# Performance work log

Measured on AMD Instinct MI355X. Metric: run time of the kernel, lower is better.

## Reference

```python
import jax, jax.numpy as jnp
import numpy as np
import math

DIM = 2048
N_HEADS = 32
N_KV_HEADS = 8
HEAD_DIM = DIM // N_HEADS  # 64
N_REP = N_HEADS // N_KV_HEADS  # 4
BSZ, SEQ = 2, 2048


def setup_inputs() -> dict:
    key = jax.random.key(0)
    ks = jax.random.split(key, 8)
    x = jax.random.normal(ks[0], (BSZ, SEQ, DIM), dtype=jnp.float32)
    # rotary tables, [seq, head_dim//2]
    inv_freq = 1.0 / (10000.0 ** (np.arange(0, HEAD_DIM, 2, dtype=np.float32) / HEAD_DIM))
    t = np.arange(SEQ, dtype=np.float32)
    freqs = np.outer(t, inv_freq)
    freqs_cos = jnp.asarray(np.cos(freqs))
    freqs_sin = jnp.asarray(np.sin(freqs))
    s = 0.02
    wq = jax.random.normal(ks[1], (DIM, N_HEADS * HEAD_DIM), dtype=jnp.float32) * s
    wk = jax.random.normal(ks[2], (DIM, N_KV_HEADS * HEAD_DIM), dtype=jnp.float32) * s
    wv = jax.random.normal(ks[3], (DIM, N_KV_HEADS * HEAD_DIM), dtype=jnp.float32) * s
    wo = jax.random.normal(ks[4], (N_HEADS * HEAD_DIM, DIM), dtype=jnp.float32) * s
    return {"x": x, "freqs_cos": freqs_cos, "freqs_sin": freqs_sin,
            "wq": wq, "wk": wk, "wv": wv, "wo": wo}


def _apply_rotary(xq, xk, cos, sin):
    # xq: [b,s,h,d], xk: [b,s,kh,d]; cos/sin: [s, d//2]
    def rot(t):
        tr = t[..., 0::2]  # even -> real
        ti = t[..., 1::2]  # odd  -> imag
        c = cos[None, :, None, :]
        s_ = sin[None, :, None, :]
        or_ = tr * c - ti * s_
        oi_ = tr * s_ + ti * c
        # interleave back: [..., d//2, 2] -> [..., d]
        return jnp.stack([or_, oi_], axis=-1).reshape(t.shape)
    return rot(xq), rot(xk)


def reference(x, freqs_cos, freqs_sin, wq, wk, wv, wo):
    b, s, _ = x.shape
    xq = (x @ wq).reshape(b, s, N_HEADS, HEAD_DIM)
    xk = (x @ wk).reshape(b, s, N_KV_HEADS, HEAD_DIM)
    xv = (x @ wv).reshape(b, s, N_KV_HEADS, HEAD_DIM)
    xq, xk = _apply_rotary(xq, xk, freqs_cos, freqs_sin)
    # repeat_kv: [b,s,kh,d] -> [b,s,kh*n_rep,d]
    xk = jnp.repeat(xk, N_REP, axis=2)
    xv = jnp.repeat(xv, N_REP, axis=2)
    # [b,h,s,d]
    q = xq.transpose(0, 2, 1, 3)
    k = xk.transpose(0, 2, 1, 3)
    v = xv.transpose(0, 2, 1, 3)
    scale = 1.0 / math.sqrt(HEAD_DIM)
    scores = jnp.einsum('bhqd,bhkd->bhqk', q, k) * scale
    causal = jnp.tril(jnp.ones((s, s), dtype=bool))
    scores = jnp.where(causal[None, None], scores, jnp.float32(-jnp.inf))
    probs = jax.nn.softmax(scores, axis=-1)
    out = jnp.einsum('bhqk,bhkd->bhqd', probs, v)  # [b,h,s,d]
    out = out.transpose(0, 2, 1, 3).reshape(b, s, N_HEADS * HEAD_DIM)
    return out @ wo
```

## Files before the change

kernel.cpp:

```cpp
#include <hip/hip_runtime.h>
#include <hip/hip_bf16.h>

typedef __attribute__((ext_vector_type(8))) short short8;
typedef __attribute__((ext_vector_type(4))) float f32x4;

__device__ __forceinline__ unsigned short f2bf(float f) {
  union { float f; unsigned u; } v; v.f = f;
  unsigned r = v.u + 0x7FFFu + ((v.u >> 16) & 1u);
  return (unsigned short)(r >> 16);
}
__device__ __forceinline__ float bf2f(unsigned short h) {
  union { unsigned u; float f; } v; v.u = ((unsigned)h) << 16;
  return v.f;
}
__device__ __forceinline__ unsigned pkbf(float a, float b) {
  __hip_bfloat162 h = __float22bfloat162_rn(float2{a, b});
  union { __hip_bfloat162 h; unsigned u; } cv; cv.h = h;
  return cv.u;
}

__global__ void prep(const float* __restrict__ x, const float* __restrict__ wq,
                     const float* __restrict__ wk, const float* __restrict__ wv,
                     const float* __restrict__ wo, unsigned short* __restrict__ xb,
                     unsigned short* __restrict__ wt, unsigned short* __restrict__ wot) {
  const int z = blockIdx.z, tid = threadIdx.x;
  if (z == 0) {
    int id = blockIdx.y * 64 + blockIdx.x;
#pragma unroll
    for (int rep = 0; rep < 2; ++rep) {
      int i = (rep * 4096 + id) * 256 + tid;
      float4 v = ((const float4*)x)[i];
      ushort4 o;
      o.x = f2bf(v.x); o.y = f2bf(v.y); o.z = f2bf(v.z); o.w = f2bf(v.w);
      ((ushort4*)xb)[i] = o;
    }
    return;
  }
  __shared__ float tile[32][33];
  const float* src;
  unsigned short* dst;
  int N;
  if (z == 1) { src = wq; dst = wt; N = 2048; }
  else if (z == 2) { src = wk; dst = wt + 2048ull * 2048; N = 512; }
  else if (z == 3) { src = wv; dst = wt + 2560ull * 2048; N = 512; }
  else { src = wo; dst = wot; N = 2048; }
  const int K = 2048;
  int n0 = blockIdx.x * 32, k0 = blockIdx.y * 32;
  if (n0 >= N) return;
  int xx = tid & 31, yy = tid >> 5;
#pragma unroll
  for (int j = 0; j < 4; ++j) tile[yy + 8 * j][xx] = src[(size_t)(k0 + yy + 8 * j) * N + n0 + xx];
  __syncthreads();
#pragma unroll
  for (int j = 0; j < 4; ++j) dst[(size_t)(n0 + yy + 8 * j) * K + k0 + xx] = f2bf(tile[xx][yy + 8 * j]);
}

template <int MODE>
__global__ __launch_bounds__(256, 2) void gemm_bt64(const unsigned short* __restrict__ A,
                                                    const unsigned short* __restrict__ Bt,
                                                    void* __restrict__ Cv, int K, int ldc,
                                                    unsigned short* __restrict__ vt,
                                                    const float* __restrict__ fcos,
                                                    const float* __restrict__ fsin) {
  __shared__ alignas(16) unsigned short As[128 * 64];
  __shared__ alignas(16) unsigned short Bs[128 * 64];
  const int t = threadIdx.x;
  const int lane = t & 63, w = t >> 6;
  const int l15 = lane & 15, quad = lane >> 4;
  const int bn0 = blockIdx.x * 128, bm0 = blockIdx.y * 128;
  const int wm = (w >> 1) * 64, wn = (w & 1) * 64;
  const unsigned short* Ab = A + (size_t)bm0 * K;
  const unsigned short* Bb = Bt + (size_t)bn0 * K;
  const int asw = l15 & 7;

  f32x4 acc[4][4];
  const f32x4 zf = {0.f, 0.f, 0.f, 0.f};
#pragma unroll
  for (int i = 0; i < 4; ++i)
#pragma unroll
    for (int j = 0; j < 4; ++j) acc[i][j] = zf;

  for (int k0 = 0; k0 < K; k0 += 64) {
    __syncthreads();
#pragma unroll
    for (int r = 0; r < 4; ++r) {
      int e = r * 256 + t;
      int row = e >> 3, cslot = e & 7;
      int cg = cslot ^ (row & 7);
      const unsigned short* ga = Ab + (size_t)row * K + k0 + cg * 8;
      __builtin_amdgcn_global_load_lds((const __attribute__((address_space(1))) void*)ga,
                                       (__attribute__((address_space(3))) void*)(As + e * 8), 16, 0, 0);
      const unsigned short* gb = Bb + (size_t)row * K + k0 + cg * 8;
      __builtin_amdgcn_global_load_lds((const __attribute__((address_space(1))) void*)gb,
                                       (__attribute__((address_space(3))) void*)(Bs + e * 8), 16, 0, 0);
    }
    __syncthreads();
#pragma unroll
    for (int s = 0; s < 2; ++s) {
      short8 af[4], bf[4];
#pragma unroll
      for (int i = 0; i < 4; ++i)
        af[i] = *reinterpret_cast<const short8*>(As + (wm + i * 16 + l15) * 64 + (((s * 4 + quad) ^ asw) * 8));
#pragma unroll
      for (int j = 0; j < 4; ++j)
        bf[j] = *reinterpret_cast<const short8*>(Bs + (wn + j * 16 + l15) * 64 + (((s * 4 + quad) ^ asw) * 8));
      __builtin_amdgcn_s_setprio(1);
#pragma unroll
      for (int i = 0; i < 4; ++i)
#pragma unroll
        for (int j = 0; j < 4; ++j)
          acc[i][j] = __builtin_amdgcn_mfma_f32_16x16x32_bf16(af[i], bf[j], acc[i][j], 0, 0, 0);
      __builtin_amdgcn_s_setprio(0);
    }
  }

  if (MODE == 1 && bn0 >= 2560) {
    const int b = bm0 >> 11;
#pragma unroll
    for (int i = 0; i < 4; ++i) {
      int srow = (bm0 + wm + i * 16 + quad * 4) & 2047;
#pragma unroll
      for (int j = 0; j < 4; ++j) {
        int vcol = bn0 - 2560 + wn + j * 16 + l15;
        int kvh = vcol >> 6, d = vcol & 63;
        uint2 pk = make_uint2(pkbf(acc[i][j][0], acc[i][j][1]), pkbf(acc[i][j][2], acc[i][j][3]));
        *reinterpret_cast<uint2*>(vt + ((size_t)(b * 8 + kvh) * 64 + d) * 2048 + srow) = pk;
      }
    }
  } else if (MODE == 1 && bn0 >= 2048) {
#pragma unroll
    for (int i = 0; i < 4; ++i)
#pragma unroll
      for (int j = 0; j < 4; ++j)
#pragma unroll
        for (int r = 0; r < 4; ++r) {
          int row = bm0 + wm + i * 16 + quad * 4 + r;
          int s = row & 2047;
          int col = bn0 + wn + j * 16 + l15;
          int fi = ((col - 2048) >> 1) & 31;
          float val = acc[i][j][r];
          float par = __shfl_xor(val, 1, 64);
          float c = fcos[s * 32 + fi], sn = fsin[s * 32 + fi];
          float o = (lane & 1) ? (par * sn + val * c) : (val * c - par * sn);
          ((unsigned short*)Cv)[(size_t)row * ldc + col] = f2bf(o);
        }
  } else {
#pragma unroll
    for (int i = 0; i < 4; ++i)
#pragma unroll
      for (int j = 0; j < 4; ++j)
#pragma unroll
        for (int r = 0; r < 4; ++r) {
          size_t row = (size_t)(bm0 + wm + i * 16 + quad * 4 + r);
          size_t col = (size_t)(bn0 + wn + j * 16 + l15);
          if (MODE == 1)
            ((unsigned short*)Cv)[row * ldc + col] = f2bf(acc[i][j][r]);
          else
            ((float*)Cv)[row * ldc + col] = acc[i][j][r];
        }
  }
}

__global__ __launch_bounds__(256, 4) void flash_attn(const unsigned short* __restrict__ qkv,
                                                     const unsigned short* __restrict__ vt,
                                                     const float* __restrict__ fcos,
                                                     const float* __restrict__ fsin,
                                                     unsigned short* __restrict__ out) {
  __shared__ alignas(16) unsigned short Ks[64 * 64];
  __shared__ alignas(16) unsigned short Vs[64 * 64];
  __shared__ alignas(16) unsigned short Ps[128 * 64];
  const int t = threadIdx.x, lane = t & 63, w = t >> 6;
  const int l15 = lane & 15, quad = lane >> 4;
  const int h = blockIdx.y, b = blockIdx.z;
  const int qb = ((int)blockIdx.x ^ (15 * (h >> 4))) & 15;
  const int q0 = qb * 128;
  const int kvh = h >> 2;
  const size_t rowB = (size_t)b * 2048;
  const unsigned short* Qg = qkv + (rowB + q0) * 2560 + h * 64;
  const unsigned short* Kg = qkv + rowB * 2560 + 2048 + kvh * 64;
  const unsigned short* Vtg = vt + (size_t)(b * 8 + kvh) * 64 * 2048;
  const float SC = 0.18033688011112042f;

  short8 qf[2][2];
#pragma unroll
  for (int mt = 0; mt < 2; ++mt)
#pragma unroll
    for (int s = 0; s < 2; ++s) {
      int qrow = w * 32 + mt * 16 + l15;
      short8 raw = *reinterpret_cast<const short8*>(Qg + (size_t)qrow * 2560 + s * 32 + quad * 8);
      f32x4 c4 = *reinterpret_cast<const f32x4*>(fcos + (size_t)(q0 + qrow) * 32 + s * 16 + quad * 4);
      f32x4 s4 = *reinterpret_cast<const f32x4*>(fsin + (size_t)(q0 + qrow) * 32 + s * 16 + quad * 4);
      short8 o;
#pragma unroll
      for (int k = 0; k < 4; ++k) {
        float xr = bf2f((unsigned short)raw[2 * k]);
        float xi = bf2f((unsigned short)raw[2 * k + 1]);
        o[2 * k] = (short)f2bf((xr * c4[k] - xi * s4[k]) * SC);
        o[2 * k + 1] = (short)f2bf((xr * s4[k] + xi * c4[k]) * SC);
      }
      qf[mt][s] = o;
    }

  const f32x4 zf = {0.f, 0.f, 0.f, 0.f};
  f32x4 oacc[2][4], lacc[2];
#pragma unroll
  for (int mt = 0; mt < 2; ++mt) {
    lacc[mt] = zf;
#pragma unroll
    for (int nt = 0; nt < 4; ++nt) oacc[mt][nt] = zf;
  }
  short8 onesf;
#pragma unroll
  for (int k = 0; k < 8; ++k) onesf[k] = (short)0x3F80;

  const int kb_end = 2 * qb + 2;
  const int srow = t >> 3, sc8 = t & 7;
  const int soff = srow * 64 + ((sc8 ^ (srow & 7)) * 8);
  const int asw = l15 & 7;
  short8 kreg[2], vreg[2];
#pragma unroll
  for (int r = 0; r < 2; ++r) {
    kreg[r] = *reinterpret_cast<const short8*>(Kg + (size_t)(srow + 32 * r) * 2560 + sc8 * 8);
    vreg[r] = *reinterpret_cast<const short8*>(Vtg + (size_t)(srow + 32 * r) * 2048 + sc8 * 8);
  }

  for (int kb = 0; kb < kb_end; ++kb) {
    __syncthreads();
#pragma unroll
    for (int r = 0; r < 2; ++r) {
      *reinterpret_cast<short8*>(Ks + soff + r * 32 * 64) = kreg[r];
      *reinterpret_cast<short8*>(Vs + soff + r * 32 * 64) = vreg[r];
    }
    __syncthreads();
    if (kb + 1 < kb_end) {
#pragma unroll
      for (int r = 0; r < 2; ++r) {
        kreg[r] = *reinterpret_cast<const short8*>(Kg + (size_t)((kb + 1) * 64 + srow + 32 * r) * 2560 + sc8 * 8);
        vreg[r] = *reinterpret_cast<const short8*>(Vtg + (size_t)(srow + 32 * r) * 2048 + (kb + 1) * 64 + sc8 * 8);
      }
    }
    const int qmaxw = q0 + w * 32 + 31;
    if (kb * 64 > qmaxw) continue;
    const bool needMask = (kb * 64 + 63) > (q0 + w * 32);

#pragma unroll
    for (int kvt = 0; kvt < 4; ++kvt) {
      f32x4 st0 = zf, st1 = zf;
#pragma unroll
      for (int s = 0; s < 2; ++s) {
        short8 kf = *reinterpret_cast<const short8*>(Ks + (kvt * 16 + l15) * 64 + ((s * 4 + quad) ^ asw) * 8);
        __builtin_amdgcn_s_setprio(1);
        st0 = __builtin_amdgcn_mfma_f32_16x16x32_bf16(kf, qf[0][s], st0, 0, 0, 0);
        st1 = __builtin_amdgcn_mfma_f32_16x16x32_bf16(kf, qf[1][s], st1, 0, 0, 0);
        __builtin_amdgcn_s_setprio(0);
      }
      const int pcol = ((kvt * 2 + (quad >> 1)) ^ asw) * 8 + (quad & 1) * 4;
      if (needMask) {
        const int kvb = kb * 64 + kvt * 16 + quad * 4;
#pragma unroll
        for (int qt = 0; qt < 2; ++qt) {
          const f32x4 stv = qt ? st1 : st0;
          const int qg = q0 + w * 32 + qt * 16 + l15;
          float p[4];
#pragma unroll
          for (int r = 0; r < 4; ++r) {
            float pv = __builtin_amdgcn_exp2f(stv[r]);
            p[r] = (kvb + r > qg) ? 0.f : pv;
          }
          *reinterpret_cast<uint2*>(Ps + (size_t)(w * 32 + qt * 16 + l15) * 64 + pcol) =
              make_uint2(pkbf(p[0], p[1]), pkbf(p[2], p[3]));
        }
      } else {
#pragma unroll
        for (int qt = 0; qt < 2; ++qt) {
          const f32x4 stv = qt ? st1 : st0;
          float p[4];
#pragma unroll
          for (int r = 0; r < 4; ++r) p[r] = __builtin_amdgcn_exp2f(stv[r]);
          *reinterpret_cast<uint2*>(Ps + (size_t)(w * 32 + qt * 16 + l15) * 64 + pcol) =
              make_uint2(pkbf(p[0], p[1]), pkbf(p[2], p[3]));
        }
      }
    }

#pragma unroll
    for (int s = 0; s < 2; ++s) {
      short8 vf[4];
#pragma unroll
      for (int nt = 0; nt < 4; ++nt)
        vf[nt] = *reinterpret_cast<const short8*>(Vs + (nt * 16 + l15) * 64 + ((s * 4 + quad) ^ asw) * 8);
#pragma unroll
      for (int mt = 0; mt < 2; ++mt) {
        short8 pf = *reinterpret_cast<const short8*>(Ps + (size_t)(w * 32 + mt * 16 + l15) * 64 + ((s * 4 + quad) ^ asw) * 8);
        __builtin_amdgcn_s_setprio(1);
#pragma unroll
        for (int nt = 0; nt < 4; ++nt)
          oacc[mt][nt] = __builtin_amdgcn_mfma_f32_16x16x32_bf16(pf, vf[nt], oacc[mt][nt], 0, 0, 0);
        lacc[mt] = __builtin_amdgcn_mfma_f32_16x16x32_bf16(pf, onesf, lacc[mt], 0, 0, 0);
        __builtin_amdgcn_s_setprio(0);
      }
    }
  }

  float linv[2][4];
#pragma unroll
  for (int mt = 0; mt < 2; ++mt)
#pragma unroll
    for (int r = 0; r < 4; ++r) linv[mt][r] = 1.f / lacc[mt][r];

#pragma unroll
  for (int mt = 0; mt < 2; ++mt)
#pragma unroll
    for (int nt = 0; nt < 4; ++nt)
#pragma unroll
      for (int r = 0; r < 4; ++r) {
        size_t row = rowB + (size_t)(q0 + w * 32 + mt * 16 + quad * 4 + r);
        size_t col = (size_t)h * 64 + nt * 16 + l15;
        out[row * 2048 + col] = f2bf(oacc[mt][nt][r] * linv[mt][r]);
      }
}

extern "C" void kernel_launch(void* const* d_in, const int* in_sizes, int n_in, void* d_out,
                              int out_size, void* d_ws, size_t ws_size, hipStream_t stream) {
  const float* x = (const float*)d_in[0];
  const float* fcos = (const float*)d_in[1];
  const float* fsin = (const float*)d_in[2];
  const float* wq = (const float*)d_in[3];
  const float* wk = (const float*)d_in[4];
  const float* wv = (const float*)d_in[5];
  const float* wo = (const float*)d_in[6];

  char* ws = (char*)d_ws;
  unsigned short* xb = (unsigned short*)ws;
  unsigned short* wt = (unsigned short*)(ws + 16777216ull);
  unsigned short* wot = (unsigned short*)(ws + 29360128ull);
  unsigned short* qkv = (unsigned short*)(ws + 37748736ull);
  unsigned short* attno = (unsigned short*)(ws + 58720256ull);
  unsigned short* vt = (unsigned short*)(ws + 75497472ull);

  prep<<<dim3(64, 64, 5), 256, 0, stream>>>(x, wq, wk, wv, wo, xb, wt, wot);
  gemm_bt64<1><<<dim3(24, 32), 256, 0, stream>>>(xb, wt, qkv, 2048, 2560, vt, fcos, fsin);
  flash_attn<<<dim3(16, 32, 2), 256, 0, stream>>>(qkv, vt, fcos, fsin, attno);
  gemm_bt64<0><<<dim3(16, 32), 256, 0, stream>>>(attno, wot, d_out, 2048, 2048, nullptr, nullptr, nullptr);
}
```

Baseline: 266.3 us.

## Rewrite projection GEMMs with triple-buffered LDS pipeline and 128x256 tiles

```diff
diff --git a/kernel.cpp b/kernel.cpp
--- a/kernel.cpp
+++ b/kernel.cpp
@@ -56,22 +56,56 @@
 }
 
 template <int MODE>
-__global__ __launch_bounds__(256, 2) void gemm_bt64(const unsigned short* __restrict__ A,
-                                                    const unsigned short* __restrict__ Bt,
-                                                    void* __restrict__ Cv, int K, int ldc,
-                                                    unsigned short* __restrict__ vt,
-                                                    const float* __restrict__ fcos,
-                                                    const float* __restrict__ fsin) {
-  __shared__ alignas(16) unsigned short As[128 * 64];
-  __shared__ alignas(16) unsigned short Bs[128 * 64];
-  const int t = threadIdx.x;
-  const int lane = t & 63, w = t >> 6;
+__global__ __launch_bounds__(512, 4) void gemm32(const unsigned short* __restrict__ A,
+                                                 const unsigned short* __restrict__ Bt,
+                                                 void* __restrict__ Cv, int K, int ldc,
+                                                 unsigned short* __restrict__ vt,
+                                                 const float* __restrict__ fcos,
+                                                 const float* __restrict__ fsin) {
+  __shared__ alignas(16) unsigned short As[3][128 * 32];
+  __shared__ alignas(16) unsigned short Bs[3][256 * 32];
+
+  const int tid = threadIdx.x;
+  const int lane = tid & 63;
+  const int w = tid >> 6;
   const int l15 = lane & 15, quad = lane >> 4;
-  const int bn0 = blockIdx.x * 128, bm0 = blockIdx.y * 128;
-  const int wm = (w >> 1) * 64, wn = (w & 1) * 64;
+  const int wr = w >> 2, wc = w & 3;
+
+  const int gx = gridDim.x;
+  int bid = blockIdx.y * gx + blockIdx.x;
+  const int nwg = gx * gridDim.y;
+  const int cpx = nwg >> 3;
+  bid = (bid & 7) * cpx + (bid >> 3);
+  const int bx = bid % gx, by = bid / gx;
+  const int bn0 = bx * 256, bm0 = by * 128;
+
   const unsigned short* Ab = A + (size_t)bm0 * K;
   const unsigned short* Bb = Bt + (size_t)bn0 * K;
-  const int asw = l15 & 7;
+
+  size_t aoffg, boffg[2];
+  int eB[2];
+  {
+    int e = tid, row = e >> 2, cs = e & 3;
+    aoffg = (size_t)row * K + (cs ^ ((row >> 1) & 3)) * 8;
+  }
+#pragma unroll
+  for (int i = 0; i < 2; ++i) {
+    int e = i * 512 + tid, row = e >> 2, cs = e & 3;
+    eB[i] = e;
+    boffg[i] = (size_t)row * K + (cs ^ ((row >> 1) & 3)) * 8;
+  }
+
+  int aoff[4], boff[4];
+#pragma unroll
+  for (int i = 0; i < 4; ++i) {
+    int R = wr * 64 + i * 16 + l15;
+    aoff[i] = R * 32 + (quad ^ ((R >> 1) & 3)) * 8;
+  }
+#pragma unroll
+  for (int j = 0; j < 4; ++j) {
+    int R = wc * 64 + j * 16 + l15;
+    boff[j] = R * 32 + (quad ^ ((R >> 1) & 3)) * 8;
+  }
 
   f32x4 acc[4][4];
   const f32x4 zf = {0.f, 0.f, 0.f, 0.f};
@@ -80,48 +114,60 @@
 #pragma unroll
     for (int j = 0; j < 4; ++j) acc[i][j] = zf;
 
-  for (int k0 = 0; k0 < K; k0 += 64) {
-    __syncthreads();
-#pragma unroll
-    for (int r = 0; r < 4; ++r) {
-      int e = r * 256 + t;
-      int row = e >> 3, cslot = e & 7;
-      int cg = cslot ^ (row & 7);
-      const unsigned short* ga = Ab + (size_t)row * K + k0 + cg * 8;
-      __builtin_amdgcn_global_load_lds((const __attribute__((address_space(1))) void*)ga,
-                                       (__attribute__((address_space(3))) void*)(As + e * 8), 16, 0, 0);
-      const unsigned short* gb = Bb + (size_t)row * K + k0 + cg * 8;
-      __builtin_amdgcn_global_load_lds((const __attribute__((address_space(1))) void*)gb,
-                                       (__attribute__((address_space(3))) void*)(Bs + e * 8), 16, 0, 0);
-    }
-    __syncthreads();
-#pragma unroll
-    for (int s = 0; s < 2; ++s) {
-      short8 af[4], bf[4];
-#pragma unroll
-      for (int i = 0; i < 4; ++i)
-        af[i] = *reinterpret_cast<const short8*>(As + (wm + i * 16 + l15) * 64 + (((s * 4 + quad) ^ asw) * 8));
+  const int NT = K >> 5;
+
+  auto stage = [&](int slot, int t) {
+    const int k0 = t * 32;
+    __builtin_amdgcn_global_load_lds(
+        (const __attribute__((address_space(1))) void*)(Ab + aoffg + k0),
+        (__attribute__((address_space(3))) void*)(&As[slot][tid * 8]), 16, 0, 0);
+#pragma unroll
+    for (int i = 0; i < 2; ++i)
+      __builtin_amdgcn_global_load_lds(
+          (const __attribute__((address_space(1))) void*)(Bb + boffg[i] + k0),
+          (__attribute__((address_space(3))) void*)(&Bs[slot][eB[i] * 8]), 16, 0, 0);
+  };
+
+  stage(0, 0);
+  stage(1, 1);
+
+  int c = 0;
+  for (int t = 0; t < NT; ++t) {
+    if (t == NT - 1) {
+      asm volatile("s_waitcnt vmcnt(0)" ::: "memory");
+    } else {
+      asm volatile("s_waitcnt vmcnt(3)" ::: "memory");
+    }
+    asm volatile("s_waitcnt lgkmcnt(0)" ::: "memory");
+    __builtin_amdgcn_s_barrier();
+    if (t + 2 < NT) {
+      int sn = c + 2; if (sn >= 3) sn -= 3;
+      stage(sn, t + 2);
+    }
+    __builtin_amdgcn_sched_barrier(0);
+    short8 af[4], bfr[4];
+#pragma unroll
+    for (int j = 0; j < 4; ++j) bfr[j] = *reinterpret_cast<const short8*>(&Bs[c][boff[j]]);
+#pragma unroll
+    for (int i = 0; i < 4; ++i) af[i] = *reinterpret_cast<const short8*>(&As[c][aoff[i]]);
+    __builtin_amdgcn_s_setprio(1);
+#pragma unroll
+    for (int i = 0; i < 4; ++i)
 #pragma unroll
       for (int j = 0; j < 4; ++j)
-        bf[j] = *reinterpret_cast<const short8*>(Bs + (wn + j * 16 + l15) * 64 + (((s * 4 + quad) ^ asw) * 8));
-      __builtin_amdgcn_s_setprio(1);
-#pragma unroll
-      for (int i = 0; i < 4; ++i)
-#pragma unroll
-        for (int j = 0; j < 4; ++j)
-          acc[i][j] = __builtin_amdgcn_mfma_f32_16x16x32_bf16(af[i], bf[j], acc[i][j], 0, 0, 0);
-      __builtin_amdgcn_s_setprio(0);
-    }
+        acc[i][j] = __builtin_amdgcn_mfma_f32_16x16x32_bf16(af[i], bfr[j], acc[i][j], 0, 0, 0);
+    __builtin_amdgcn_s_setprio(0);
+    c = (c == 2) ? 0 : c + 1;
   }
 
   if (MODE == 1 && bn0 >= 2560) {
     const int b = bm0 >> 11;
 #pragma unroll
     for (int i = 0; i < 4; ++i) {
-      int srow = (bm0 + wm + i * 16 + quad * 4) & 2047;
+      int srow = (bm0 + wr * 64 + i * 16 + quad * 4) & 2047;
 #pragma unroll
       for (int j = 0; j < 4; ++j) {
-        int vcol = bn0 - 2560 + wn + j * 16 + l15;
+        int vcol = bn0 - 2560 + wc * 64 + j * 16 + l15;
         int kvh = vcol >> 6, d = vcol & 63;
         uint2 pk = make_uint2(pkbf(acc[i][j][0], acc[i][j][1]), pkbf(acc[i][j][2], acc[i][j][3]));
         *reinterpret_cast<uint2*>(vt + ((size_t)(b * 8 + kvh) * 64 + d) * 2048 + srow) = pk;
@@ -134,14 +180,14 @@
       for (int j = 0; j < 4; ++j)
 #pragma unroll
         for (int r = 0; r < 4; ++r) {
-          int row = bm0 + wm + i * 16 + quad * 4 + r;
+          int row = bm0 + wr * 64 + i * 16 + quad * 4 + r;
           int s = row & 2047;
-          int col = bn0 + wn + j * 16 + l15;
+          int col = bn0 + wc * 64 + j * 16 + l15;
           int fi = ((col - 2048) >> 1) & 31;
           float val = acc[i][j][r];
           float par = __shfl_xor(val, 1, 64);
-          float c = fcos[s * 32 + fi], sn = fsin[s * 32 + fi];
-          float o = (lane & 1) ? (par * sn + val * c) : (val * c - par * sn);
+          float cth = fcos[s * 32 + fi], sn = fsin[s * 32 + fi];
+          float o = (lane & 1) ? (par * sn + val * cth) : (val * cth - par * sn);
           ((unsigned short*)Cv)[(size_t)row * ldc + col] = f2bf(o);
         }
   } else {
@@ -151,8 +197,8 @@
       for (int j = 0; j < 4; ++j)
 #pragma unroll
         for (int r = 0; r < 4; ++r) {
-          size_t row = (size_t)(bm0 + wm + i * 16 + quad * 4 + r);
-          size_t col = (size_t)(bn0 + wn + j * 16 + l15);
+          size_t row = (size_t)(bm0 + wr * 64 + i * 16 + quad * 4 + r);
+          size_t col = (size_t)(bn0 + wc * 64 + j * 16 + l15);
           if (MODE == 1)
             ((unsigned short*)Cv)[row * ldc + col] = f2bf(acc[i][j][r]);
           else
@@ -339,7 +385,7 @@
   unsigned short* vt = (unsigned short*)(ws + 75497472ull);
 
   prep<<<dim3(64, 64, 5), 256, 0, stream>>>(x, wq, wk, wv, wo, xb, wt, wot);
-  gemm_bt64<1><<<dim3(24, 32), 256, 0, stream>>>(xb, wt, qkv, 2048, 2560, vt, fcos, fsin);
+  gemm32<1><<<dim3(12, 32), 512, 0, stream>>>(xb, wt, qkv, 2048, 2560, vt, fcos, fsin);
   flash_attn<<<dim3(16, 32, 2), 256, 0, stream>>>(qkv, vt, fcos, fsin, attno);
-  gemm_bt64<0><<<dim3(16, 32), 256, 0, stream>>>(attno, wot, d_out, 2048, 2048, nullptr, nullptr, nullptr);
-}
+  gemm32<0><<<dim3(8, 32), 512, 0, stream>>>(attno, wot, d_out, 2048, 2048, nullptr, nullptr, nullptr);
+}
```

Result: slower. 298.5 us (+12.1%).

## Pair early and late 64-row query tiles per block to balance causal attention work

Applied to the files above, without the earlier changes.

```diff
diff --git a/kernel.cpp b/kernel.cpp
--- a/kernel.cpp
+++ b/kernel.cpp
@@ -172,24 +172,27 @@
   const int t = threadIdx.x, lane = t & 63, w = t >> 6;
   const int l15 = lane & 15, quad = lane >> 4;
   const int h = blockIdx.y, b = blockIdx.z;
-  const int qb = ((int)blockIdx.x ^ (15 * (h >> 4))) & 15;
-  const int q0 = qb * 128;
+  const int tp = ((int)blockIdx.x ^ (h & 15)) & 15;
+  const int qA0 = tp * 64;
+  const int qB0 = (31 - tp) * 64;
   const int kvh = h >> 2;
   const size_t rowB = (size_t)b * 2048;
-  const unsigned short* Qg = qkv + (rowB + q0) * 2560 + h * 64;
   const unsigned short* Kg = qkv + rowB * 2560 + 2048 + kvh * 64;
   const unsigned short* Vtg = vt + (size_t)(b * 8 + kvh) * 64 * 2048;
   const float SC = 0.18033688011112042f;
 
+  const int qbase0 = qA0 + w * 16;
+  const int qbase1 = qB0 + w * 16;
+
   short8 qf[2][2];
 #pragma unroll
-  for (int mt = 0; mt < 2; ++mt)
+  for (int mt = 0; mt < 2; ++mt) {
+    const int qrow = (mt ? qbase1 : qbase0) + l15;
 #pragma unroll
     for (int s = 0; s < 2; ++s) {
-      int qrow = w * 32 + mt * 16 + l15;
-      short8 raw = *reinterpret_cast<const short8*>(Qg + (size_t)qrow * 2560 + s * 32 + quad * 8);
-      f32x4 c4 = *reinterpret_cast<const f32x4*>(fcos + (size_t)(q0 + qrow) * 32 + s * 16 + quad * 4);
-      f32x4 s4 = *reinterpret_cast<const f32x4*>(fsin + (size_t)(q0 + qrow) * 32 + s * 16 + quad * 4);
+      short8 raw = *reinterpret_cast<const short8*>(qkv + (rowB + qrow) * 2560 + h * 64 + s * 32 + quad * 8);
+      f32x4 c4 = *reinterpret_cast<const f32x4*>(fcos + (size_t)qrow * 32 + s * 16 + quad * 4);
+      f32x4 s4 = *reinterpret_cast<const f32x4*>(fsin + (size_t)qrow * 32 + s * 16 + quad * 4);
       short8 o;
 #pragma unroll
       for (int k = 0; k < 4; ++k) {
@@ -200,6 +203,7 @@
       }
       qf[mt][s] = o;
     }
+  }
 
   const f32x4 zf = {0.f, 0.f, 0.f, 0.f};
   f32x4 oacc[2][4], lacc[2];
@@ -213,7 +217,7 @@
 #pragma unroll
   for (int k = 0; k < 8; ++k) onesf[k] = (short)0x3F80;
 
-  const int kb_end = 2 * qb + 2;
+  const int kb_end = 32 - tp;
   const int srow = t >> 3, sc8 = t & 7;
   const int soff = srow * 64 + ((sc8 ^ (srow & 7)) * 8);
   const int asw = l15 & 7;
@@ -239,9 +243,9 @@
         vreg[r] = *reinterpret_cast<const short8*>(Vtg + (size_t)(srow + 32 * r) * 2048 + (kb + 1) * 64 + sc8 * 8);
       }
     }
-    const int qmaxw = q0 + w * 32 + 31;
-    if (kb * 64 > qmaxw) continue;
-    const bool needMask = (kb * 64 + 63) > (q0 + w * 32);
+    const bool actA = (kb <= tp);
+    const bool mA = (kb == tp);
+    const bool mB = (kb == kb_end - 1);
 
 #pragma unroll
     for (int kvt = 0; kvt < 4; ++kvt) {
@@ -250,36 +254,43 @@
       for (int s = 0; s < 2; ++s) {
         short8 kf = *reinterpret_cast<const short8*>(Ks + (kvt * 16 + l15) * 64 + ((s * 4 + quad) ^ asw) * 8);
         __builtin_amdgcn_s_setprio(1);
-        st0 = __builtin_amdgcn_mfma_f32_16x16x32_bf16(kf, qf[0][s], st0, 0, 0, 0);
+        if (actA) st0 = __builtin_amdgcn_mfma_f32_16x16x32_bf16(kf, qf[0][s], st0, 0, 0, 0);
         st1 = __builtin_amdgcn_mfma_f32_16x16x32_bf16(kf, qf[1][s], st1, 0, 0, 0);
         __builtin_amdgcn_s_setprio(0);
       }
       const int pcol = ((kvt * 2 + (quad >> 1)) ^ asw) * 8 + (quad & 1) * 4;
-      if (needMask) {
-        const int kvb = kb * 64 + kvt * 16 + quad * 4;
-#pragma unroll
-        for (int qt = 0; qt < 2; ++qt) {
-          const f32x4 stv = qt ? st1 : st0;
-          const int qg = q0 + w * 32 + qt * 16 + l15;
-          float p[4];
+      const int kvb = kb * 64 + kvt * 16 + quad * 4;
+      if (actA) {
+        float p[4];
+        if (mA) {
+          const int qg = qbase0 + l15;
 #pragma unroll
           for (int r = 0; r < 4; ++r) {
-            float pv = __builtin_amdgcn_exp2f(stv[r]);
+            float pv = __builtin_amdgcn_exp2f(st0[r]);
             p[r] = (kvb + r > qg) ? 0.f : pv;
           }
-          *reinterpret_cast<uint2*>(Ps + (size_t)(w * 32 + qt * 16 + l15) * 64 + pcol) =
-              make_uint2(pkbf(p[0], p[1]), pkbf(p[2], p[3]));
+        } else {
+#pragma unroll
+          for (int r = 0; r < 4; ++r) p[r] = __builtin_amdgcn_exp2f(st0[r]);
         }
-      } else {
-#pragma unroll
-        for (int qt = 0; qt < 2; ++qt) {
-          const f32x4 stv = qt ? st1 : st0;
-          float p[4];
-#pragma unroll
-          for (int r = 0; r < 4; ++r) p[r] = __builtin_amdgcn_exp2f(stv[r]);
-          *reinterpret_cast<uint2*>(Ps + (size_t)(w * 32 + qt * 16 + l15) * 64 + pcol) =
-              make_uint2(pkbf(p[0], p[1]), pkbf(p[2], p[3]));
+        *reinterpret_cast<uint2*>(Ps + (size_t)(w * 32 + l15) * 64 + pcol) =
+            make_uint2(pkbf(p[0], p[1]), pkbf(p[2], p[3]));
+      }
+      {
+        float p[4];
+        if (mB) {
+          const int qg = qbase1 + l15;
+#pragma unroll
+          for (int r = 0; r < 4; ++r) {
+            float pv = __builtin_amdgcn_exp2f(st1[r]);
+            p[r] = (kvb + r > qg) ? 0.f : pv;
+          }
+        } else {
+#pragma unroll
+          for (int r = 0; r < 4; ++r) p[r] = __builtin_amdgcn_exp2f(st1[r]);
         }
+        *reinterpret_cast<uint2*>(Ps + (size_t)(w * 32 + 16 + l15) * 64 + pcol) =
+            make_uint2(pkbf(p[0], p[1]), pkbf(p[2], p[3]));
       }
     }
 
@@ -291,6 +302,7 @@
         vf[nt] = *reinterpret_cast<const short8*>(Vs + (nt * 16 + l15) * 64 + ((s * 4 + quad) ^ asw) * 8);
 #pragma unroll
       for (int mt = 0; mt < 2; ++mt) {
+        if (mt == 0 && !actA) continue;
         short8 pf = *reinterpret_cast<const short8*>(Ps + (size_t)(w * 32 + mt * 16 + l15) * 64 + ((s * 4 + quad) ^ asw) * 8);
         __builtin_amdgcn_s_setprio(1);
 #pragma unroll
@@ -309,15 +321,17 @@
     for (int r = 0; r < 4; ++r) linv[mt][r] = 1.f / lacc[mt][r];
 
 #pragma unroll
-  for (int mt = 0; mt < 2; ++mt)
+  for (int mt = 0; mt < 2; ++mt) {
+    const int base = mt ? qbase1 : qbase0;
 #pragma unroll
     for (int nt = 0; nt < 4; ++nt)
 #pragma unroll
       for (int r = 0; r < 4; ++r) {
-        size_t row = rowB + (size_t)(q0 + w * 32 + mt * 16 + quad * 4 + r);
+        size_t row = rowB + (size_t)(base + quad * 4 + r);
         size_t col = (size_t)h * 64 + nt * 16 + l15;
         out[row * 2048 + col] = f2bf(oacc[mt][nt][r] * linv[mt][r]);
       }
+  }
 }
 
 extern "C" void kernel_launch(void* const* d_in, const int* in_sizes, int n_in, void* d_out,
```

After: 322.6 us. 21.2% more time.

## Read K/V fragments directly from global memory in flash attention, drop LDS staging

Applied to the files above, without the earlier changes.

```diff
diff --git a/kernel.cpp b/kernel.cpp
--- a/kernel.cpp
+++ b/kernel.cpp
@@ -166,19 +166,20 @@
                                                      const float* __restrict__ fcos,
                                                      const float* __restrict__ fsin,
                                                      unsigned short* __restrict__ out) {
-  __shared__ alignas(16) unsigned short Ks[64 * 64];
-  __shared__ alignas(16) unsigned short Vs[64 * 64];
   __shared__ alignas(16) unsigned short Ps[128 * 64];
   const int t = threadIdx.x, lane = t & 63, w = t >> 6;
   const int l15 = lane & 15, quad = lane >> 4;
-  const int h = blockIdx.y, b = blockIdx.z;
-  const int qb = ((int)blockIdx.x ^ (15 * (h >> 4))) & 15;
+  const int hs = blockIdx.x;
+  const int h = ((hs & 7) << 2) + (hs >> 3);
+  const int yy = blockIdx.y;
+  const int qb = (yy < 8) ? yy : 23 - yy;
+  const int b = blockIdx.z;
   const int q0 = qb * 128;
-  const int kvh = h >> 2;
+  const int kvh = hs & 7;
   const size_t rowB = (size_t)b * 2048;
   const unsigned short* Qg = qkv + (rowB + q0) * 2560 + h * 64;
-  const unsigned short* Kg = qkv + rowB * 2560 + 2048 + kvh * 64;
-  const unsigned short* Vtg = vt + (size_t)(b * 8 + kvh) * 64 * 2048;
+  const unsigned short* Kgb = qkv + rowB * 2560 + 2048 + kvh * 64;
+  const unsigned short* Vgb = vt + (size_t)(b * 8 + kvh) * 64 * 2048;
   const float SC = 0.18033688011112042f;
 
   short8 qf[2][2];
@@ -213,42 +214,19 @@
 #pragma unroll
   for (int k = 0; k < 8; ++k) onesf[k] = (short)0x3F80;
 
-  const int kb_end = 2 * qb + 2;
-  const int srow = t >> 3, sc8 = t & 7;
-  const int soff = srow * 64 + ((sc8 ^ (srow & 7)) * 8);
   const int asw = l15 & 7;
-  short8 kreg[2], vreg[2];
-#pragma unroll
-  for (int r = 0; r < 2; ++r) {
-    kreg[r] = *reinterpret_cast<const short8*>(Kg + (size_t)(srow + 32 * r) * 2560 + sc8 * 8);
-    vreg[r] = *reinterpret_cast<const short8*>(Vtg + (size_t)(srow + 32 * r) * 2048 + sc8 * 8);
-  }
+  const int kb_end = 2 * qb + 1 + (w >> 1);
 
   for (int kb = 0; kb < kb_end; ++kb) {
-    __syncthreads();
-#pragma unroll
-    for (int r = 0; r < 2; ++r) {
-      *reinterpret_cast<short8*>(Ks + soff + r * 32 * 64) = kreg[r];
-      *reinterpret_cast<short8*>(Vs + soff + r * 32 * 64) = vreg[r];
-    }
-    __syncthreads();
-    if (kb + 1 < kb_end) {
-#pragma unroll
-      for (int r = 0; r < 2; ++r) {
-        kreg[r] = *reinterpret_cast<const short8*>(Kg + (size_t)((kb + 1) * 64 + srow + 32 * r) * 2560 + sc8 * 8);
-        vreg[r] = *reinterpret_cast<const short8*>(Vtg + (size_t)(srow + 32 * r) * 2048 + (kb + 1) * 64 + sc8 * 8);
-      }
-    }
-    const int qmaxw = q0 + w * 32 + 31;
-    if (kb * 64 > qmaxw) continue;
     const bool needMask = (kb * 64 + 63) > (q0 + w * 32);
 
 #pragma unroll
     for (int kvt = 0; kvt < 4; ++kvt) {
       f32x4 st0 = zf, st1 = zf;
+      const unsigned short* Kr = Kgb + (size_t)(kb * 64 + kvt * 16 + l15) * 2560;
 #pragma unroll
       for (int s = 0; s < 2; ++s) {
-        short8 kf = *reinterpret_cast<const short8*>(Ks + (kvt * 16 + l15) * 64 + ((s * 4 + quad) ^ asw) * 8);
+        short8 kf = *reinterpret_cast<const short8*>(Kr + (s * 4 + quad) * 8);
         __builtin_amdgcn_s_setprio(1);
         st0 = __builtin_amdgcn_mfma_f32_16x16x32_bf16(kf, qf[0][s], st0, 0, 0, 0);
         st1 = __builtin_amdgcn_mfma_f32_16x16x32_bf16(kf, qf[1][s], st1, 0, 0, 0);
@@ -288,7 +266,7 @@
       short8 vf[4];
 #pragma unroll
       for (int nt = 0; nt < 4; ++nt)
-        vf[nt] = *reinterpret_cast<const short8*>(Vs + (nt * 16 + l15) * 64 + ((s * 4 + quad) ^ asw) * 8);
+        vf[nt] = *reinterpret_cast<const short8*>(Vgb + (size_t)(nt * 16 + l15) * 2048 + kb * 64 + (s * 4 + quad) * 8);
 #pragma unroll
       for (int mt = 0; mt < 2; ++mt) {
         short8 pf = *reinterpret_cast<const short8*>(Ps + (size_t)(w * 32 + mt * 16 + l15) * 64 + ((s * 4 + quad) ^ asw) * 8);
@@ -340,6 +318,6 @@
 
   prep<<<dim3(64, 64, 5), 256, 0, stream>>>(x, wq, wk, wv, wo, xb, wt, wot);
   gemm_bt64<1><<<dim3(24, 32), 256, 0, stream>>>(xb, wt, qkv, 2048, 2560, vt, fcos, fsin);
-  flash_attn<<<dim3(16, 32, 2), 256, 0, stream>>>(qkv, vt, fcos, fsin, attno);
+  flash_attn<<<dim3(32, 16, 2), 256, 0, stream>>>(qkv, vt, fcos, fsin, attno);
   gemm_bt64<0><<<dim3(16, 32), 256, 0, stream>>>(attno, wot, d_out, 2048, 2048, nullptr, nullptr, nullptr);
 }
```

After: 355.5 us. 33.5% more time.
